# Performance work log

Hardware: AMD Instinct MI355X
Metric: run time of the kernel (lower is better)

The kernel has to match this reference:

```python
import jax, jax.numpy as jnp
import numpy as np

N, C, D = 8192, 21, 5


def setup_inputs() -> dict:
    key = jax.random.key(0)
    k1, k2 = jax.random.split(key)
    U = jax.random.normal(k1, (N, C), dtype=jnp.float32)
    ref = jax.random.normal(k2, (N, D), dtype=jnp.float32)
    return {"U": U, "ref": ref}


def reference(U, ref):
    # Exact Gaussian lattice filter: out_i = sum_j exp(-||f_i - f_j||^2 / 2) U_j - U_i
    # (the permutohedral lattice is an approximation of this kernel matvec).
    sq = jnp.sum(ref * ref, axis=-1)                      # [N]
    # pairwise squared distances: ||f_i||^2 + ||f_j||^2 - 2 f_i.f_j
    d2 = sq[:, None] + sq[None, :] - 2.0 * (ref @ ref.T)  # [N, N]
    W = jnp.exp(-0.5 * jnp.maximum(d2, 0.0))              # [N, N] Gaussian kernel
    return W @ U - U                                      # (W - I) @ U
```

## Files before the change

kernel.cpp:

```cpp
#include <hip/hip_runtime.h>
#include <hip/hip_bf16.h>


#define NN 8192
#define CC 21
#define DD 5
#define NTILE_G (NN / 32)
#define ROWS 32
#define NBLK (NN / ROWS)
#define MAINT 1024
#define NWAVE 16
#define TPW (NTILE_G / NWAVE)

#define F_OFF 0
#define U_OFF (NTILE_G * 64 * 16)

typedef __attribute__((ext_vector_type(8)))  short    bf16x8;
typedef __attribute__((ext_vector_type(16))) float    f32x16;
typedef __attribute__((ext_vector_type(4)))  unsigned u32x4;

__device__ __forceinline__ short bf16s(float x) {
    __hip_bfloat16 h = __float2bfloat16(x);
    short s; __builtin_memcpy(&s, &h, 2); return s;
}
__device__ __forceinline__ float bf16f(short s) {
    __hip_bfloat16 h; __builtin_memcpy(&h, &s, 2); return __bfloat162float(h);
}

__global__ __launch_bounds__(256)
void pack_frags(const float* __restrict__ U, const float* __restrict__ ref,
                char* __restrict__ ws) {
    const int q = blockIdx.x * 256 + threadIdx.x;
    if (q < NTILE_G * 64) {
        const int tile = q >> 6, ln = q & 63;
        const int j = tile * 32 + (ln & 31);
        const float* fj = ref + (size_t)j * DD;
        short h_[5], l_[5];
        #pragma unroll
        for (int d = 0; d < DD; ++d) {
            const float f = fj[d];
            h_[d] = bf16s(f);
            l_[d] = bf16s(f - bf16f(h_[d]));
        }
        short v[8] __attribute__((aligned(16)));
        if (ln < 32) {
            v[0]=h_[0]; v[1]=h_[1]; v[2]=h_[2]; v[3]=h_[3];
            v[4]=h_[4]; v[5]=l_[0]; v[6]=l_[1]; v[7]=l_[2];
        } else {
            v[0]=l_[3]; v[1]=l_[4]; v[2]=h_[0]; v[3]=h_[1];
            v[4]=h_[2]; v[5]=h_[3]; v[6]=h_[4]; v[7]=0;
        }
        u32x4 pk; __builtin_memcpy(&pk, v, 16);
        *(u32x4*)(ws + F_OFF + (size_t)q * 16) = pk;
    } else {
        const int qu = q - NTILE_G * 64;
        const int ln = qu & 63, kt = (qu >> 6) & 1, tile = qu >> 7;
        const int c = ln & 31, g = ln >> 5;
        short v[8] __attribute__((aligned(16))) = {0,0,0,0,0,0,0,0};
        if (c < CC) {
            #pragma unroll
            for (int e = 0; e < 8; ++e) {
                const int j = tile * 32 + kt * 16 + (e & 3) + 8 * (e >> 2) + 4 * g;
                v[e] = bf16s(U[(size_t)j * CC + c]);
            }
        }
        u32x4 pk; __builtin_memcpy(&pk, v, 16);
        *(u32x4*)(ws + U_OFF + (size_t)qu * 16) = pk;
    }
}

__global__ __launch_bounds__(MAINT, 4)
void lattice_main(const float* __restrict__ U, const float* __restrict__ ref,
                  const char* __restrict__ ws, float* __restrict__ out) {
    __shared__ __align__(16) char smem[65536];
    float* ajb = (float*)smem;
    float* red = (float*)smem;

    const int t    = threadIdx.x;
    const int lane = t & 63;
    const int wv   = t >> 6;
    const int h    = lane >> 5;
    const int m    = lane & 31;
    const int ibase = blockIdx.x * ROWS;
    const float L  = 1.4426950408889634f;
    const float NH = -0.7213475204444817f;

    for (int j = t; j < NN; j += MAINT) {
        const float* fj = ref + (size_t)j * DD;
        const float f0 = fj[0], f1 = fj[1], f2 = fj[2], f3 = fj[3], f4 = fj[4];
        ajb[j] = NH * (f0*f0 + f1*f1 + f2*f2 + f3*f3 + f4*f4);
    }

    const float* fiP = ref + (size_t)(ibase + m) * DD;
    const float fi0 = fiP[0], fi1 = fiP[1], fi2 = fiP[2], fi3 = fiP[3], fi4 = fiP[4];
    const float ai = NH * (fi0*fi0 + fi1*fi1 + fi2*fi2 + fi3*fi3 + fi4*fi4);
    bf16x8 bfi;
    {
        const float sf[5] = {L*fi0, L*fi1, L*fi2, L*fi3, L*fi4};
        short hi_[5], lo_[5];
        #pragma unroll
        for (int d = 0; d < DD; ++d) {
            hi_[d] = bf16s(sf[d]);
            lo_[d] = bf16s(sf[d] - bf16f(hi_[d]));
        }
        short bv[8] __attribute__((aligned(16)));
        bv[0] = h ? hi_[3] : hi_[0];
        bv[1] = h ? hi_[4] : hi_[1];
        bv[2] = h ? lo_[0] : hi_[2];
        bv[3] = h ? lo_[1] : hi_[3];
        bv[4] = h ? lo_[2] : hi_[4];
        bv[5] = h ? lo_[3] : hi_[0];
        bv[6] = h ? lo_[4] : hi_[1];
        bv[7] = h ? (short)0 : hi_[2];
        __builtin_memcpy(&bfi, bv, 16);
    }

    f32x16 acc;
    #pragma unroll
    for (int r = 0; r < 16; ++r) acc[r] = 0.f;

    __syncthreads();

    const char* Fws = ws + F_OFF;
    const char* Uws = ws + U_OFF;

    #pragma unroll 2
    for (int s = 0; s < TPW; ++s) {
        const int tile = wv * TPW + s;
        const u32x4 fr = *(const u32x4*)(Fws + ((size_t)(tile * 64 + lane)) * 16);
        const u32x4 b0 = *(const u32x4*)(Uws + ((size_t)((tile * 2 + 0) * 64 + lane)) * 16);
        const u32x4 b1 = *(const u32x4*)(Uws + ((size_t)((tile * 2 + 1) * 64 + lane)) * 16);

        f32x16 sacc;
        #pragma unroll
        for (int r = 0; r < 16; ++r) sacc[r] = 0.f;
        sacc = __builtin_amdgcn_mfma_f32_32x32x16_bf16(
            __builtin_bit_cast(bf16x8, fr), bfi, sacc, 0, 0, 0);

        const float* ajp = ajb + tile * 32 + 4 * h;
        float aqf[16] __attribute__((aligned(16)));
        *(float4*)&aqf[0]  = *(const float4*)(ajp);
        *(float4*)&aqf[4]  = *(const float4*)(ajp + 8);
        *(float4*)&aqf[8]  = *(const float4*)(ajp + 16);
        *(float4*)&aqf[12] = *(const float4*)(ajp + 24);

        short wv16[16] __attribute__((aligned(16)));
        #pragma unroll
        for (int r = 0; r < 16; ++r) {
            float x = (ai + aqf[r]) + sacc[r];
            x = fminf(x, 0.f);
            wv16[r] = bf16s(__builtin_amdgcn_exp2f(x));
        }
        bf16x8 a0, a1;
        __builtin_memcpy(&a0, &wv16[0], 16);
        __builtin_memcpy(&a1, &wv16[8], 16);

        acc = __builtin_amdgcn_mfma_f32_32x32x16_bf16(
            a0, __builtin_bit_cast(bf16x8, b0), acc, 0, 0, 0);
        acc = __builtin_amdgcn_mfma_f32_32x32x16_bf16(
            a1, __builtin_bit_cast(bf16x8, b1), acc, 0, 0, 0);
    }

    __syncthreads();

    #pragma unroll
    for (int r = 0; r < 16; ++r) {
        const int row = (r & 3) + 8 * (r >> 2) + 4 * h;
        red[wv * 1024 + row * 32 + m] = acc[r];
    }
    __syncthreads();

    {
        const int row = t >> 5, col = t & 31;
        float s = 0.f;
        #pragma unroll
        for (int w = 0; w < NWAVE; ++w) s += red[w * 1024 + row * 32 + col];
        if (col < CC) {
            const size_t o = (size_t)(ibase + row) * CC + col;
            out[o] = s - U[o];
        }
    }
}

extern "C" void kernel_launch(void* const* d_in, const int* in_sizes, int n_in,
                              void* d_out, int out_size, void* d_ws, size_t ws_size,
                              hipStream_t stream) {
    const float* U   = (const float*)d_in[0];
    const float* ref = (const float*)d_in[1];
    float* out = (float*)d_out;
    char* ws = (char*)d_ws;

    const int pack_threads = NTILE_G * 64 + NTILE_G * 2 * 64;
    pack_frags<<<pack_threads / 256, 256, 0, stream>>>(U, ref, ws);
    lattice_main<<<NBLK, MAINT, 0, stream>>>(U, ref, (const char*)ws, out);
}
```

Baseline: 26.60 us.

## Fold squared-norm term into MFMA and split j-range across blocks with atomics

Packs the -|f_j|^2/2 term as bf16 hi/lo pairs into the feature fragment and pairs them with ones in the row operand, so the distance MFMA yields the full exponent directly. This drops the shared-memory norm table, its fill loop, an early barrier and the clamp. The j dimension is split four ways across a 2D grid of smaller 512-thread blocks, with partial sums combined by atomic adds into an output cleared by a memset first. Removing the clamp lets small positive exponents through, the bf16 split of the norm may lose some precision, and the change adds a memset and atomic traffic.

```diff
diff --git a/kernel.cpp b/kernel.cpp
--- a/kernel.cpp
+++ b/kernel.cpp
@@ -7,10 +7,12 @@
 #define DD 5
 #define NTILE_G (NN / 32)
 #define ROWS 32
-#define NBLK (NN / ROWS)
-#define MAINT 1024
-#define NWAVE 16
-#define TPW (NTILE_G / NWAVE)
+#define NIB (NN / ROWS)
+#define JSPLIT 4
+#define TPB (NTILE_G / JSPLIT)
+#define BLOCK 512
+#define NWAVE 8
+#define TPW (TPB / NWAVE)
 
 #define F_OFF 0
 #define U_OFF (NTILE_G * 64 * 16)
@@ -30,25 +32,31 @@
 __global__ __launch_bounds__(256)
 void pack_frags(const float* __restrict__ U, const float* __restrict__ ref,
                 char* __restrict__ ws) {
+    const float NH = -0.7213475204444817f;
     const int q = blockIdx.x * 256 + threadIdx.x;
     if (q < NTILE_G * 64) {
         const int tile = q >> 6, ln = q & 63;
         const int j = tile * 32 + (ln & 31);
         const float* fj = ref + (size_t)j * DD;
         short h_[5], l_[5];
+        float sq = 0.f;
         #pragma unroll
         for (int d = 0; d < DD; ++d) {
             const float f = fj[d];
+            sq = fmaf(f, f, sq);
             h_[d] = bf16s(f);
             l_[d] = bf16s(f - bf16f(h_[d]));
         }
+        const float a = NH * sq;
+        const short ajh = bf16s(a);
+        const short ajl = bf16s(a - bf16f(ajh));
         short v[8] __attribute__((aligned(16)));
         if (ln < 32) {
             v[0]=h_[0]; v[1]=h_[1]; v[2]=h_[2]; v[3]=h_[3];
             v[4]=h_[4]; v[5]=l_[0]; v[6]=l_[1]; v[7]=l_[2];
         } else {
             v[0]=l_[3]; v[1]=l_[4]; v[2]=h_[0]; v[3]=h_[1];
-            v[4]=h_[2]; v[5]=h_[3]; v[6]=h_[4]; v[7]=0;
+            v[4]=h_[2]; v[5]=ajh;   v[6]=ajl;   v[7]=h_[3];
         }
         u32x4 pk; __builtin_memcpy(&pk, v, 16);
         *(u32x4*)(ws + F_OFF + (size_t)q * 16) = pk;
@@ -69,12 +77,10 @@
     }
 }
 
-__global__ __launch_bounds__(MAINT, 4)
+__global__ __launch_bounds__(BLOCK, 8)
 void lattice_main(const float* __restrict__ U, const float* __restrict__ ref,
                   const char* __restrict__ ws, float* __restrict__ out) {
-    __shared__ __align__(16) char smem[65536];
-    float* ajb = (float*)smem;
-    float* red = (float*)smem;
+    __shared__ __align__(16) float red[NWAVE * ROWS * 32];
 
     const int t    = threadIdx.x;
     const int lane = t & 63;
@@ -82,14 +88,9 @@
     const int h    = lane >> 5;
     const int m    = lane & 31;
     const int ibase = blockIdx.x * ROWS;
+    const int jc    = blockIdx.y;
     const float L  = 1.4426950408889634f;
     const float NH = -0.7213475204444817f;
-
-    for (int j = t; j < NN; j += MAINT) {
-        const float* fj = ref + (size_t)j * DD;
-        const float f0 = fj[0], f1 = fj[1], f2 = fj[2], f3 = fj[3], f4 = fj[4];
-        ajb[j] = NH * (f0*f0 + f1*f1 + f2*f2 + f3*f3 + f4*f4);
-    }
 
     const float* fiP = ref + (size_t)(ibase + m) * DD;
     const float fi0 = fiP[0], fi1 = fiP[1], fi2 = fiP[2], fi3 = fiP[3], fi4 = fiP[4];
@@ -103,15 +104,16 @@
             hi_[d] = bf16s(sf[d]);
             lo_[d] = bf16s(sf[d] - bf16f(hi_[d]));
         }
+        const short one = bf16s(1.0f);
         short bv[8] __attribute__((aligned(16)));
         bv[0] = h ? hi_[3] : hi_[0];
         bv[1] = h ? hi_[4] : hi_[1];
         bv[2] = h ? lo_[0] : hi_[2];
         bv[3] = h ? lo_[1] : hi_[3];
         bv[4] = h ? lo_[2] : hi_[4];
-        bv[5] = h ? lo_[3] : hi_[0];
-        bv[6] = h ? lo_[4] : hi_[1];
-        bv[7] = h ? (short)0 : hi_[2];
+        bv[5] = h ? one    : hi_[0];
+        bv[6] = h ? one    : hi_[1];
+        bv[7] = h ? lo_[3] : hi_[2];
         __builtin_memcpy(&bfi, bv, 16);
     }
 
@@ -119,14 +121,12 @@
     #pragma unroll
     for (int r = 0; r < 16; ++r) acc[r] = 0.f;
 
-    __syncthreads();
-
     const char* Fws = ws + F_OFF;
     const char* Uws = ws + U_OFF;
+    const int tile0 = jc * TPB + wv * TPW;
 
-    #pragma unroll 2
     for (int s = 0; s < TPW; ++s) {
-        const int tile = wv * TPW + s;
+        const int tile = tile0 + s;
         const u32x4 fr = *(const u32x4*)(Fws + ((size_t)(tile * 64 + lane)) * 16);
         const u32x4 b0 = *(const u32x4*)(Uws + ((size_t)((tile * 2 + 0) * 64 + lane)) * 16);
         const u32x4 b1 = *(const u32x4*)(Uws + ((size_t)((tile * 2 + 1) * 64 + lane)) * 16);
@@ -137,20 +137,10 @@
         sacc = __builtin_amdgcn_mfma_f32_32x32x16_bf16(
             __builtin_bit_cast(bf16x8, fr), bfi, sacc, 0, 0, 0);
 
-        const float* ajp = ajb + tile * 32 + 4 * h;
-        float aqf[16] __attribute__((aligned(16)));
-        *(float4*)&aqf[0]  = *(const float4*)(ajp);
-        *(float4*)&aqf[4]  = *(const float4*)(ajp + 8);
-        *(float4*)&aqf[8]  = *(const float4*)(ajp + 16);
-        *(float4*)&aqf[12] = *(const float4*)(ajp + 24);
-
         short wv16[16] __attribute__((aligned(16)));
         #pragma unroll
-        for (int r = 0; r < 16; ++r) {
-            float x = (ai + aqf[r]) + sacc[r];
-            x = fminf(x, 0.f);
-            wv16[r] = bf16s(__builtin_amdgcn_exp2f(x));
-        }
+        for (int r = 0; r < 16; ++r)
+            wv16[r] = bf16s(__builtin_amdgcn_exp2f(ai + sacc[r]));
         bf16x8 a0, a1;
         __builtin_memcpy(&a0, &wv16[0], 16);
         __builtin_memcpy(&a1, &wv16[8], 16);
@@ -161,23 +151,24 @@
             a1, __builtin_bit_cast(bf16x8, b1), acc, 0, 0, 0);
     }
 
+    #pragma unroll
+    for (int r = 0; r < 16; ++r) {
+        const int row = (r & 3) + 8 * (r >> 2) + 4 * h;
+        red[wv * (ROWS * 32) + row * 32 + m] = acc[r];
+    }
     __syncthreads();
 
     #pragma unroll
-    for (int r = 0; r < 16; ++r) {
-        const int row = (r & 3) + 8 * (r >> 2) + 4 * h;
-        red[wv * 1024 + row * 32 + m] = acc[r];
-    }
-    __syncthreads();
-
-    {
-        const int row = t >> 5, col = t & 31;
+    for (int k = 0; k < 2; ++k) {
+        const int idx = k * BLOCK + t;
+        const int row = idx >> 5, col = idx & 31;
         float s = 0.f;
         #pragma unroll
-        for (int w = 0; w < NWAVE; ++w) s += red[w * 1024 + row * 32 + col];
+        for (int w = 0; w < NWAVE; ++w) s += red[w * (ROWS * 32) + row * 32 + col];
         if (col < CC) {
             const size_t o = (size_t)(ibase + row) * CC + col;
-            out[o] = s - U[o];
+            if (jc == 0) s -= U[o];
+            unsafeAtomicAdd(&out[o], s);
         }
     }
 }
@@ -190,7 +181,11 @@
     float* out = (float*)d_out;
     char* ws = (char*)d_ws;
 
+    hipMemsetAsync(out, 0, (size_t)out_size * sizeof(float), stream);
+
     const int pack_threads = NTILE_G * 64 + NTILE_G * 2 * 64;
     pack_frags<<<pack_threads / 256, 256, 0, stream>>>(U, ref, ws);
-    lattice_main<<<NBLK, MAINT, 0, stream>>>(U, ref, (const char*)ws, out);
+
+    dim3 grid(NIB, JSPLIT);
+    lattice_main<<<grid, BLOCK, 0, stream>>>(U, ref, (const char*)ws, out);
 }
```

New measurement: 25.05 us. 1.06x faster.
